# Performance work log

Measured on AMD Instinct MI355X. Metric: run time of the kernel, lower is better.

Reference implementation:

```python
import jax, jax.numpy as jnp
import numpy as np

N, E, G, L = 100000, 1600000, 2000, 2000
IN, H1, H2, H3, OUT = 128, 64, 32, 16, 16
EPS = 1e-5


def _layernorm(x, g, b):
    m = jnp.mean(x, axis=-1, keepdims=True)
    v = jnp.mean(jnp.square(x - m), axis=-1, keepdims=True)
    return (x - m) * jax.lax.rsqrt(v + EPS) * g + b


def _gcn_block(x, W, b, Wr, br, g, beta, src, dst, deg_inv_sqrt):
    # GCNConv with added self-loops and symmetric normalization (PyG default)
    h = x @ W  # [N, F]
    coef = (deg_inv_sqrt[src] * deg_inv_sqrt[dst])[:, None]  # [E, 1]
    msg = h[src] * coef  # [E, F] -- dominant memory traffic
    agg = jax.ops.segment_sum(msg, dst, num_segments=N)
    agg = agg + h * jnp.square(deg_inv_sqrt)[:, None] + b  # self-loop term + bias
    out = agg + (x @ Wr + br)  # residual projection
    return jax.nn.relu(_layernorm(out, g, beta))


def setup_inputs():
    key = jax.random.key(0)
    ks = jax.random.split(key, 40)
    w = lambda k, i, o: jax.random.normal(k, (i, o), jnp.float32) / np.sqrt(i)
    d = {}
    d['x'] = jax.random.normal(ks[0], (N, IN), jnp.float32)
    d['src'] = jax.random.randint(ks[1], (E,), 0, N, jnp.int32)
    d['dst'] = jax.random.randint(ks[2], (E,), 0, N, jnp.int32)
    d['batch'] = jnp.sort(jax.random.randint(ks[3], (N,), 0, G, jnp.int32))
    d['link_idx'] = jax.random.randint(ks[4], (2, L), 0, G, jnp.int32)
    dims = [(IN, H1), (H1, H2), (H2, H3), (H3, OUT)]
    for i, (fi, fo) in enumerate(dims, 1):
        d[f'W{i}'] = w(ks[5 + 4 * i], fi, fo)
        d[f'b{i}'] = jnp.zeros((fo,), jnp.float32)
        d[f'Wr{i}'] = w(ks[6 + 4 * i], fi, fo)
        d[f'br{i}'] = jnp.zeros((fo,), jnp.float32)
        d[f'g{i}'] = jnp.ones((fo,), jnp.float32)
        d[f'bt{i}'] = jnp.zeros((fo,), jnp.float32)
    d['Wm1'] = w(ks[30], 2 * OUT, OUT)
    d['bm1'] = jnp.zeros((OUT,), jnp.float32)
    d['Wm2'] = w(ks[31], OUT, OUT // 2)
    d['bm2'] = jnp.zeros((OUT // 2,), jnp.float32)
    d['Wm3'] = w(ks[32], OUT // 2, 1)
    d['bm3'] = jnp.zeros((1,), jnp.float32)
    return d


def reference(x, src, dst, batch, link_idx,
              W1, b1, Wr1, br1, g1, bt1,
              W2, b2, Wr2, br2, g2, bt2,
              W3, b3, Wr3, br3, g3, bt3,
              W4, b4, Wr4, br4, g4, bt4,
              Wm1, bm1, Wm2, bm2, Wm3, bm3):
    ones_e = jnp.ones((E,), jnp.float32)
    deg = jax.ops.segment_sum(ones_e, dst, num_segments=N) + 1.0  # + self-loop
    dis = jax.lax.rsqrt(deg)
    h = _gcn_block(x, W1, b1, Wr1, br1, g1, bt1, src, dst, dis)
    h = _gcn_block(h, W2, b2, Wr2, br2, g2, bt2, src, dst, dis)
    h = _gcn_block(h, W3, b3, Wr3, br3, g3, bt3, src, dst, dis)
    h = _gcn_block(h, W4, b4, Wr4, br4, g4, bt4, src, dst, dis)
    # global mean pool over subgraphs
    cnt = jax.ops.segment_sum(jnp.ones((N,), jnp.float32), batch, num_segments=G)
    gemb = jax.ops.segment_sum(h, batch, num_segments=G) / jnp.maximum(cnt, 1.0)[:, None]
    feat = jnp.concatenate([gemb[link_idx[0]], gemb[link_idx[1]]], axis=1)  # [L, 2*OUT]
    z = jax.nn.relu(feat @ Wm1 + bm1)
    z = jax.nn.relu(z @ Wm2 + bm2)
    z = z @ Wm3 + bm3
    return jax.nn.sigmoid(z).squeeze(-1)  # [L]
```

## Files before the change

kernel.cpp:

```cpp
#include <hip/hip_runtime.h>
#include <math.h>

namespace {

constexpr int N = 100000;
constexpr int E = 1600000;
constexpr int G = 2000;
constexpr int L = 2000;

constexpr int SCAN_CHUNK = 1024;
constexpr int NB = (N + SCAN_CHUNK - 1) / SCAN_CHUNK;

constexpr int NXCD = 8;
constexpr int NP = N / NXCD;

__device__ __forceinline__ float bf2f(unsigned short u) {
  union { unsigned int i; float f; } v;
  v.i = ((unsigned int)u) << 16;
  return v.f;
}
__device__ __forceinline__ unsigned short f2bf(float f) {
  union { float f; unsigned int i; } v;
  v.f = f;
  const unsigned int x = v.i;
  return (unsigned short)((x + 0x7FFFu + ((x >> 16) & 1u)) >> 16);
}


__global__ void hist_part_kernel(const int* __restrict__ dst, int* __restrict__ deg) {
  const int part = blockIdx.x & (NXCD - 1);
  const int lo = part * NP;
  const int hi = lo + NP;
  const int bidp = blockIdx.x >> 3;
  const int stridev = (gridDim.x >> 3) * blockDim.x;
  const int nvec = E >> 2;
  for (int v = bidp * blockDim.x + threadIdx.x; v < nvec; v += stridev) {
    const int4 d4 = *reinterpret_cast<const int4*>(dst + v * 4);
    if (d4.x >= lo && d4.x < hi) atomicAdd(&deg[d4.x], 1);
    if (d4.y >= lo && d4.y < hi) atomicAdd(&deg[d4.y], 1);
    if (d4.z >= lo && d4.z < hi) atomicAdd(&deg[d4.z], 1);
    if (d4.w >= lo && d4.w < hi) atomicAdd(&deg[d4.w], 1);
  }
}

__global__ void fill_part_kernel(const int* __restrict__ src, const int* __restrict__ dst,
                                 int* __restrict__ cursor, int* __restrict__ col) {
  const int part = blockIdx.x & (NXCD - 1);
  const int lo = part * NP;
  const int hi = lo + NP;
  const int bidp = blockIdx.x >> 3;
  const int stridev = (gridDim.x >> 3) * blockDim.x;
  const int nvec = E >> 2;
  for (int v = bidp * blockDim.x + threadIdx.x; v < nvec; v += stridev) {
    const int e = v * 4;
    const int4 d4 = *reinterpret_cast<const int4*>(dst + e);
    if (d4.x >= lo && d4.x < hi) col[atomicAdd(&cursor[d4.x], 1)] = src[e];
    if (d4.y >= lo && d4.y < hi) col[atomicAdd(&cursor[d4.y], 1)] = src[e + 1];
    if (d4.z >= lo && d4.z < hi) col[atomicAdd(&cursor[d4.z], 1)] = src[e + 2];
    if (d4.w >= lo && d4.w < hi) col[atomicAdd(&cursor[d4.w], 1)] = src[e + 3];
  }
}

__global__ void scan1_kernel(const int* __restrict__ deg, int* __restrict__ bsum) {
  const int t = threadIdx.x;
  const int base = blockIdx.x * SCAN_CHUNK + t * 4;
  int s = 0;
  if (base < N) {
    const int4 v = *reinterpret_cast<const int4*>(deg + base);
    s = v.x + v.y + v.z + v.w;
  }
  __shared__ int ss[256];
  ss[t] = s;
  __syncthreads();
#pragma unroll
  for (int off = 128; off >= 1; off >>= 1) {
    if (t < off) ss[t] += ss[t + off];
    __syncthreads();
  }
  if (t == 0) bsum[blockIdx.x] = ss[0];
}

__global__ void scan2_kernel(const int* __restrict__ bsum, int* __restrict__ boff) {
  __shared__ int ss[128];
  const int t = threadIdx.x;
  ss[t] = (t < NB) ? bsum[t] : 0;
  __syncthreads();
#pragma unroll
  for (int off = 1; off < 128; off <<= 1) {
    int v = (t >= off) ? ss[t - off] : 0;
    __syncthreads();
    ss[t] += v;
    __syncthreads();
  }
  if (t < NB) boff[t] = (t == 0) ? 0 : ss[t - 1];
}

__global__ void scan3_kernel(const int* __restrict__ deg, const int* __restrict__ boff,
                             int* __restrict__ row_ptr, int* __restrict__ cursor,
                             float* __restrict__ dis) {
  const int t = threadIdx.x;
  const int base = blockIdx.x * SCAN_CHUNK + t * 4;
  int d0 = 0, d1 = 0, d2 = 0, d3 = 0;
  if (base < N) {
    const int4 v = *reinterpret_cast<const int4*>(deg + base);
    d0 = v.x; d1 = v.y; d2 = v.z; d3 = v.w;
  }
  const int tsum = d0 + d1 + d2 + d3;
  __shared__ int ss[256];
  ss[t] = tsum;
  __syncthreads();
#pragma unroll
  for (int off = 1; off < 256; off <<= 1) {
    int v = (t >= off) ? ss[t - off] : 0;
    __syncthreads();
    ss[t] += v;
    __syncthreads();
  }
  if (base < N) {
    const int p0 = ((t == 0) ? 0 : ss[t - 1]) + boff[blockIdx.x];
    const int p1 = p0 + d0;
    const int p2 = p1 + d1;
    const int p3 = p2 + d2;
    *reinterpret_cast<int4*>(row_ptr + base) = make_int4(p0, p1, p2, p3);
    *reinterpret_cast<int4*>(cursor + base) = make_int4(p0, p1, p2, p3);
    const float4 dv = make_float4(rsqrtf((float)d0 + 1.0f), rsqrtf((float)d1 + 1.0f),
                                  rsqrtf((float)d2 + 1.0f), rsqrtf((float)d3 + 1.0f));
    *reinterpret_cast<float4*>(dis + base) = dv;
  }
  if (blockIdx.x == 0 && t == 0) row_ptr[N] = E;
}


__device__ __forceinline__ void f4fma(float4& a, float s, const float4 w) {
  a.x = fmaf(s, w.x, a.x);
  a.y = fmaf(s, w.y, a.y);
  a.z = fmaf(s, w.z, a.z);
  a.w = fmaf(s, w.w, a.w);
}

template <int FI, int FO>
__global__ __launch_bounds__(1024) void gemm2_kernel(const float* __restrict__ x,
                                                     const float* __restrict__ W,
                                                     const float* __restrict__ Wr,
                                                     const float* __restrict__ dis,
                                                     unsigned short* __restrict__ hdb,
                                                     float* __restrict__ r) {
  __shared__ float sW[FI * FO];
  __shared__ float sWr[FI * FO];
  for (int i = threadIdx.x; i < FI * FO; i += blockDim.x) {
    sW[i] = W[i];
    sWr[i] = Wr[i];
  }
  __syncthreads();
  constexpr int CG = FO / 4;
  const int total = (N / 4) * CG;
  const int stride = gridDim.x * blockDim.x;
  for (int idx = blockIdx.x * blockDim.x + threadIdx.x; idx < total; idx += stride) {
    const int rb = idx / CG;
    const int col = (idx - rb * CG) * 4;
    const int row0 = rb * 4;
    float4 aH[4], aR[4];
#pragma unroll
    for (int i = 0; i < 4; ++i) {
      aH[i] = make_float4(0.f, 0.f, 0.f, 0.f);
      aR[i] = make_float4(0.f, 0.f, 0.f, 0.f);
    }
    const float* xr = x + (size_t)row0 * FI;
#pragma unroll
    for (int k = 0; k < FI; k += 4) {
      float xs[4][4];
#pragma unroll
      for (int i = 0; i < 4; ++i) {
        const float4 xv = *reinterpret_cast<const float4*>(xr + i * FI + k);
        xs[i][0] = xv.x; xs[i][1] = xv.y; xs[i][2] = xv.z; xs[i][3] = xv.w;
      }
#pragma unroll
      for (int kk = 0; kk < 4; ++kk) {
        const float4 w4 = *reinterpret_cast<const float4*>(&sW[(k + kk) * FO + col]);
        const float4 w4r = *reinterpret_cast<const float4*>(&sWr[(k + kk) * FO + col]);
#pragma unroll
        for (int i = 0; i < 4; ++i) {
          f4fma(aH[i], xs[i][kk], w4);
          f4fma(aR[i], xs[i][kk], w4r);
        }
      }
    }
    const float4 dv = *reinterpret_cast<const float4*>(dis + row0);
    const float dl[4] = {dv.x, dv.y, dv.z, dv.w};
#pragma unroll
    for (int i = 0; i < 4; ++i) {
      ushort4 ob;
      ob.x = f2bf(aH[i].x * dl[i]);
      ob.y = f2bf(aH[i].y * dl[i]);
      ob.z = f2bf(aH[i].z * dl[i]);
      ob.w = f2bf(aH[i].w * dl[i]);
      *reinterpret_cast<ushort4*>(&hdb[(size_t)(row0 + i) * FO + col]) = ob;
      *reinterpret_cast<float4*>(&r[(size_t)(row0 + i) * FO + col]) = aR[i];
    }
  }
}


template <int FO, bool POOL>
__global__ void gcn_agg_kernel(const int* __restrict__ row_ptr, const int* __restrict__ col,
                               const unsigned short* __restrict__ hdb, const float* __restrict__ r,
                               const float* __restrict__ dis,
                               const float* __restrict__ b, const float* __restrict__ br,
                               const float* __restrict__ g, const float* __restrict__ bt,
                               float* __restrict__ out, const int* __restrict__ batch,
                               float* __restrict__ gemb, float* __restrict__ cnt) {
  constexpr int NPW = 64 / FO;
  const int lane = threadIdx.x & 63;
  const int f = lane & (FO - 1);
  const int sub = lane / FO;
  const int waveId = (blockIdx.x * blockDim.x + threadIdx.x) >> 6;
  const int nWaves = (gridDim.x * blockDim.x) >> 6;
  const int nGroups = N / NPW;
  const float bf = b[f], brf = br[f], gf = g[f], btf = bt[f];
  for (int w = waveId; w < nGroups; w += nWaves) {
    const int node = w * NPW + sub;
    const int beg = row_ptr[node];
    const int end = row_ptr[node + 1];
    float a0 = 0.f, a1 = 0.f, a2 = 0.f, a3 = 0.f;
    int k = beg;
    const int end4 = beg + ((end - beg) & ~3);
    for (; k < end4; k += 4) {
      const int s0 = col[k];
      const int s1 = col[k + 1];
      const int s2 = col[k + 2];
      const int s3 = col[k + 3];
      a0 += bf2f(hdb[(size_t)s0 * FO + f]);
      a1 += bf2f(hdb[(size_t)s1 * FO + f]);
      a2 += bf2f(hdb[(size_t)s2 * FO + f]);
      a3 += bf2f(hdb[(size_t)s3 * FO + f]);
    }
    for (; k < end; ++k) a0 += bf2f(hdb[(size_t)col[k] * FO + f]);
    const float acc = (a0 + a1) + (a2 + a3);
    const float dv = dis[node];
    const size_t base = (size_t)node * FO + f;
    const float v = fmaf(dv, acc + bf2f(hdb[base]), bf + r[base] + brf);
    float s = v;
#pragma unroll
    for (int m = FO / 2; m >= 1; m >>= 1) s += __shfl_xor(s, m, 64);
    const float mean = s * (1.0f / FO);
    const float d0 = v - mean;
    float vs = d0 * d0;
#pragma unroll
    for (int m = FO / 2; m >= 1; m >>= 1) vs += __shfl_xor(vs, m, 64);
    const float var = vs * (1.0f / FO);
    float o = d0 * rsqrtf(var + 1e-5f) * gf + btf;
    o = fmaxf(o, 0.f);
    if (POOL) {
      const int bb = batch[node];
      atomicAdd(&gemb[bb * FO + f], o);
      if (f == 0) atomicAdd(&cnt[bb], 1.0f);
    } else {
      out[base] = o;
    }
  }
}


__global__ void gdiv_kernel(float* __restrict__ gemb, const float* __restrict__ cnt) {
  const int idx = blockIdx.x * blockDim.x + threadIdx.x;
  if (idx < G * 16) gemb[idx] /= fmaxf(cnt[idx >> 4], 1.0f);
}

__global__ void mlp_kernel(const float* __restrict__ gemb, const int* __restrict__ link,
                           const float* __restrict__ Wm1, const float* __restrict__ bm1,
                           const float* __restrict__ Wm2, const float* __restrict__ bm2,
                           const float* __restrict__ Wm3, const float* __restrict__ bm3,
                           float* __restrict__ out) {
  __shared__ float sW1[32 * 16], sW2[16 * 8], sW3[8], sb1[16], sb2[8], sb3;
  for (int i = threadIdx.x; i < 32 * 16; i += blockDim.x) sW1[i] = Wm1[i];
  for (int i = threadIdx.x; i < 16 * 8; i += blockDim.x) sW2[i] = Wm2[i];
  if (threadIdx.x < 8) {
    sW3[threadIdx.x] = Wm3[threadIdx.x];
    sb2[threadIdx.x] = bm2[threadIdx.x];
  }
  if (threadIdx.x < 16) sb1[threadIdx.x] = bm1[threadIdx.x];
  if (threadIdx.x == 0) sb3 = bm3[0];
  __syncthreads();
  const int l = blockIdx.x * blockDim.x + threadIdx.x;
  if (l >= L) return;
  const int a = link[l];
  const int c = link[L + l];
  float feat[32];
#pragma unroll
  for (int k = 0; k < 16; ++k) feat[k] = gemb[a * 16 + k];
#pragma unroll
  for (int k = 0; k < 16; ++k) feat[16 + k] = gemb[c * 16 + k];
  float z1[16];
#pragma unroll
  for (int j = 0; j < 16; ++j) {
    float s = sb1[j];
#pragma unroll
    for (int k = 0; k < 32; ++k) s = fmaf(feat[k], sW1[k * 16 + j], s);
    z1[j] = fmaxf(s, 0.f);
  }
  float z2[8];
#pragma unroll
  for (int j = 0; j < 8; ++j) {
    float s = sb2[j];
#pragma unroll
    for (int k = 0; k < 16; ++k) s = fmaf(z1[k], sW2[k * 8 + j], s);
    z2[j] = fmaxf(s, 0.f);
  }
  float z3 = sb3;
#pragma unroll
  for (int k = 0; k < 8; ++k) z3 = fmaf(z2[k], sW3[k], z3);
  out[l] = 1.f / (1.f + expf(-z3));
}

}

extern "C" void kernel_launch(void* const* d_in, const int* in_sizes, int n_in,
                              void* d_out, int out_size, void* d_ws, size_t ws_size,
                              hipStream_t stream) {
  (void)in_sizes; (void)n_in; (void)out_size; (void)ws_size;
  const float* x = (const float*)d_in[0];
  const int* src = (const int*)d_in[1];
  const int* dst = (const int*)d_in[2];
  const int* batch = (const int*)d_in[3];
  const int* link = (const int*)d_in[4];
  const float *Wl[4], *bl[4], *Wrl[4], *brl[4], *gl[4], *btl[4];
  for (int i = 0; i < 4; ++i) {
    Wl[i] = (const float*)d_in[5 + 6 * i + 0];
    bl[i] = (const float*)d_in[5 + 6 * i + 1];
    Wrl[i] = (const float*)d_in[5 + 6 * i + 2];
    brl[i] = (const float*)d_in[5 + 6 * i + 3];
    gl[i] = (const float*)d_in[5 + 6 * i + 4];
    btl[i] = (const float*)d_in[5 + 6 * i + 5];
  }
  const float* Wm1 = (const float*)d_in[29];
  const float* bm1 = (const float*)d_in[30];
  const float* Wm2 = (const float*)d_in[31];
  const float* bm2 = (const float*)d_in[32];
  const float* Wm3 = (const float*)d_in[33];
  const float* bm3 = (const float*)d_in[34];
  float* out = (float*)d_out;

  char* wsb = (char*)d_ws;
  int* deg_i = (int*)wsb;
  int* row_ptr = deg_i + N;
  int* cursor = row_ptr + (N + 1);
  float* dis = (float*)(cursor + N);
  int* bsum = (int*)(dis + N);
  int* boff = bsum + NB;
  int* col = boff + NB;
  unsigned short* hdb = (unsigned short*)(col + E);
  float* bufB = (float*)(hdb + (size_t)N * 64);
  float* bufC = bufB + (size_t)N * 64;
  float* gemb = bufC + (size_t)N * 64;
  float* cnt = gemb + (size_t)G * 16;

  hipMemsetAsync(deg_i, 0, N * sizeof(int), stream);
  hist_part_kernel<<<2048, 256, 0, stream>>>(dst, deg_i);
  scan1_kernel<<<NB, 256, 0, stream>>>(deg_i, bsum);
  scan2_kernel<<<1, 128, 0, stream>>>(bsum, boff);
  scan3_kernel<<<NB, 256, 0, stream>>>(deg_i, boff, row_ptr, cursor, dis);
  fill_part_kernel<<<2048, 256, 0, stream>>>(src, dst, cursor, col);

  const int AGG_BLOCKS = 2048;

  gemm2_kernel<128, 64><<<((N / 4) * 16 + 1023) / 1024, 1024, 0, stream>>>(x, Wl[0], Wrl[0], dis, hdb, bufB);
  gcn_agg_kernel<64, false><<<AGG_BLOCKS, 256, 0, stream>>>(row_ptr, col, hdb, bufB, dis,
                                                            bl[0], brl[0], gl[0], btl[0], bufC,
                                                            batch, gemb, cnt);
  gemm2_kernel<64, 32><<<((N / 4) * 8 + 1023) / 1024, 1024, 0, stream>>>(bufC, Wl[1], Wrl[1], dis, hdb, bufB);
  gcn_agg_kernel<32, false><<<AGG_BLOCKS, 256, 0, stream>>>(row_ptr, col, hdb, bufB, dis,
                                                            bl[1], brl[1], gl[1], btl[1], bufC,
                                                            batch, gemb, cnt);
  gemm2_kernel<32, 16><<<((N / 4) * 4 + 1023) / 1024, 1024, 0, stream>>>(bufC, Wl[2], Wrl[2], dis, hdb, bufB);
  gcn_agg_kernel<16, false><<<AGG_BLOCKS, 256, 0, stream>>>(row_ptr, col, hdb, bufB, dis,
                                                            bl[2], brl[2], gl[2], btl[2], bufC,
                                                            batch, gemb, cnt);
  hipMemsetAsync(gemb, 0, (size_t)(G * 16 + G) * sizeof(float), stream);
  gemm2_kernel<16, 16><<<((N / 4) * 4 + 1023) / 1024, 1024, 0, stream>>>(bufC, Wl[3], Wrl[3], dis, hdb, bufB);
  gcn_agg_kernel<16, true><<<AGG_BLOCKS, 256, 0, stream>>>(row_ptr, col, hdb, bufB, dis,
                                                           bl[3], brl[3], gl[3], btl[3], nullptr,
                                                           batch, gemb, cnt);
  gdiv_kernel<<<(G * 16 + 255) / 256, 256, 0, stream>>>(gemb, cnt);
  mlp_kernel<<<(L + 255) / 256, 256, 0, stream>>>(gemb, link, Wm1, bm1, Wm2, bm2, Wm3, bm3, out);
}
```

Measured before the change: 628.3 us.

## Fuse scan kernels cooperatively, fold pool zeroing and divide, unroll gather by 8

Merges the three-stage degree scan into one cooperative kernel that uses grid syncs, and moves the pool-buffer memset into the last GEMM kernel. It also folds the mean-pool division into the MLP kernel, removing several launches. Separately, the aggregation gather loop is unrolled to 8 with clamped indices and predicated adds, putting more loads in flight. The cooperative launch and grid syncs add their own overhead, and the clamped loads issue redundant memory reads for the tail of each neighbour list.

```diff
diff --git a/kernel.cpp b/kernel.cpp
--- a/kernel.cpp
+++ b/kernel.cpp
@@ -1,5 +1,8 @@
 #include <hip/hip_runtime.h>
+#include <hip/hip_cooperative_groups.h>
 #include <math.h>
+
+namespace cg = cooperative_groups;
 
 namespace {
 
@@ -61,63 +64,60 @@
   }
 }
 
-__global__ void scan1_kernel(const int* __restrict__ deg, int* __restrict__ bsum) {
-  const int t = threadIdx.x;
-  const int base = blockIdx.x * SCAN_CHUNK + t * 4;
-  int s = 0;
-  if (base < N) {
-    const int4 v = *reinterpret_cast<const int4*>(deg + base);
-    s = v.x + v.y + v.z + v.w;
-  }
+__global__ __launch_bounds__(256) void scan_fused_kernel(const int* __restrict__ deg,
+                                                         int* __restrict__ bsum,
+                                                         int* __restrict__ boff,
+                                                         int* __restrict__ row_ptr,
+                                                         int* __restrict__ cursor,
+                                                         float* __restrict__ dis) {
+  cg::grid_group grid = cg::this_grid();
+  const int tid = threadIdx.x;
+  const int bid = blockIdx.x;
+  const int base = bid * SCAN_CHUNK + tid * 4;
   __shared__ int ss[256];
-  ss[t] = s;
-  __syncthreads();
-#pragma unroll
-  for (int off = 128; off >= 1; off >>= 1) {
-    if (t < off) ss[t] += ss[t + off];
-    __syncthreads();
-  }
-  if (t == 0) bsum[blockIdx.x] = ss[0];
-}
-
-__global__ void scan2_kernel(const int* __restrict__ bsum, int* __restrict__ boff) {
-  __shared__ int ss[128];
-  const int t = threadIdx.x;
-  ss[t] = (t < NB) ? bsum[t] : 0;
-  __syncthreads();
-#pragma unroll
-  for (int off = 1; off < 128; off <<= 1) {
-    int v = (t >= off) ? ss[t - off] : 0;
-    __syncthreads();
-    ss[t] += v;
-    __syncthreads();
-  }
-  if (t < NB) boff[t] = (t == 0) ? 0 : ss[t - 1];
-}
-
-__global__ void scan3_kernel(const int* __restrict__ deg, const int* __restrict__ boff,
-                             int* __restrict__ row_ptr, int* __restrict__ cursor,
-                             float* __restrict__ dis) {
-  const int t = threadIdx.x;
-  const int base = blockIdx.x * SCAN_CHUNK + t * 4;
+
   int d0 = 0, d1 = 0, d2 = 0, d3 = 0;
   if (base < N) {
     const int4 v = *reinterpret_cast<const int4*>(deg + base);
     d0 = v.x; d1 = v.y; d2 = v.z; d3 = v.w;
   }
-  const int tsum = d0 + d1 + d2 + d3;
-  __shared__ int ss[256];
-  ss[t] = tsum;
+  ss[tid] = d0 + d1 + d2 + d3;
   __syncthreads();
 #pragma unroll
+  for (int off = 128; off >= 1; off >>= 1) {
+    if (tid < off) ss[tid] += ss[tid + off];
+    __syncthreads();
+  }
+  if (tid == 0) bsum[bid] = ss[0];
+  grid.sync();
+
+  if (bid == 0) {
+    __shared__ int s2[256];
+    s2[tid] = (tid < NB) ? bsum[tid] : 0;
+    __syncthreads();
+#pragma unroll
+    for (int off = 1; off < 256; off <<= 1) {
+      const int v = (tid >= off) ? s2[tid - off] : 0;
+      __syncthreads();
+      s2[tid] += v;
+      __syncthreads();
+    }
+    if (tid < NB) boff[tid] = (tid == 0) ? 0 : s2[tid - 1];
+  }
+  grid.sync();
+
+  __syncthreads();
+  ss[tid] = d0 + d1 + d2 + d3;
+  __syncthreads();
+#pragma unroll
   for (int off = 1; off < 256; off <<= 1) {
-    int v = (t >= off) ? ss[t - off] : 0;
+    const int v = (tid >= off) ? ss[tid - off] : 0;
     __syncthreads();
-    ss[t] += v;
+    ss[tid] += v;
     __syncthreads();
   }
   if (base < N) {
-    const int p0 = ((t == 0) ? 0 : ss[t - 1]) + boff[blockIdx.x];
+    const int p0 = ((tid == 0) ? 0 : ss[tid - 1]) + boff[bid];
     const int p1 = p0 + d0;
     const int p2 = p1 + d1;
     const int p3 = p2 + d2;
@@ -127,7 +127,7 @@
                                   rsqrtf((float)d2 + 1.0f), rsqrtf((float)d3 + 1.0f));
     *reinterpret_cast<float4*>(dis + base) = dv;
   }
-  if (blockIdx.x == 0 && t == 0) row_ptr[N] = E;
+  if (bid == 0 && tid == 0) row_ptr[N] = E;
 }
 
 
@@ -138,18 +138,24 @@
   a.w = fmaf(s, w.w, a.w);
 }
 
-template <int FI, int FO>
+template <int FI, int FO, bool ZERO_POOL>
 __global__ __launch_bounds__(1024) void gemm2_kernel(const float* __restrict__ x,
                                                      const float* __restrict__ W,
                                                      const float* __restrict__ Wr,
                                                      const float* __restrict__ dis,
                                                      unsigned short* __restrict__ hdb,
-                                                     float* __restrict__ r) {
+                                                     float* __restrict__ r,
+                                                     float* __restrict__ gemb_cnt) {
   __shared__ float sW[FI * FO];
   __shared__ float sWr[FI * FO];
   for (int i = threadIdx.x; i < FI * FO; i += blockDim.x) {
     sW[i] = W[i];
     sWr[i] = Wr[i];
+  }
+  if (ZERO_POOL) {
+    const int gstride = gridDim.x * blockDim.x;
+    for (int i = blockIdx.x * blockDim.x + threadIdx.x; i < G * 16 + G; i += gstride)
+      gemb_cnt[i] = 0.f;
   }
   __syncthreads();
   constexpr int CG = FO / 4;
@@ -221,21 +227,31 @@
     const int node = w * NPW + sub;
     const int beg = row_ptr[node];
     const int end = row_ptr[node + 1];
-    float a0 = 0.f, a1 = 0.f, a2 = 0.f, a3 = 0.f;
-    int k = beg;
-    const int end4 = beg + ((end - beg) & ~3);
-    for (; k < end4; k += 4) {
-      const int s0 = col[k];
-      const int s1 = col[k + 1];
-      const int s2 = col[k + 2];
-      const int s3 = col[k + 3];
-      a0 += bf2f(hdb[(size_t)s0 * FO + f]);
-      a1 += bf2f(hdb[(size_t)s1 * FO + f]);
-      a2 += bf2f(hdb[(size_t)s2 * FO + f]);
-      a3 += bf2f(hdb[(size_t)s3 * FO + f]);
-    }
-    for (; k < end; ++k) a0 += bf2f(hdb[(size_t)col[k] * FO + f]);
-    const float acc = (a0 + a1) + (a2 + a3);
+    float a0 = 0.f, a1 = 0.f, a2 = 0.f, a3 = 0.f, a4 = 0.f, a5 = 0.f, a6 = 0.f, a7 = 0.f;
+    for (int k = beg; k < end; k += 8) {
+      const int e1 = end - 1;
+      const int k0 = k, k1 = min(k + 1, e1), k2 = min(k + 2, e1), k3 = min(k + 3, e1);
+      const int k4 = min(k + 4, e1), k5 = min(k + 5, e1), k6 = min(k + 6, e1), k7 = min(k + 7, e1);
+      const int s0 = col[k0], s1 = col[k1], s2 = col[k2], s3 = col[k3];
+      const int s4 = col[k4], s5 = col[k5], s6 = col[k6], s7 = col[k7];
+      const float v0 = bf2f(hdb[(size_t)s0 * FO + f]);
+      const float v1 = bf2f(hdb[(size_t)s1 * FO + f]);
+      const float v2 = bf2f(hdb[(size_t)s2 * FO + f]);
+      const float v3 = bf2f(hdb[(size_t)s3 * FO + f]);
+      const float v4 = bf2f(hdb[(size_t)s4 * FO + f]);
+      const float v5 = bf2f(hdb[(size_t)s5 * FO + f]);
+      const float v6 = bf2f(hdb[(size_t)s6 * FO + f]);
+      const float v7 = bf2f(hdb[(size_t)s7 * FO + f]);
+      a0 += v0;
+      a1 += (k + 1 < end) ? v1 : 0.f;
+      a2 += (k + 2 < end) ? v2 : 0.f;
+      a3 += (k + 3 < end) ? v3 : 0.f;
+      a4 += (k + 4 < end) ? v4 : 0.f;
+      a5 += (k + 5 < end) ? v5 : 0.f;
+      a6 += (k + 6 < end) ? v6 : 0.f;
+      a7 += (k + 7 < end) ? v7 : 0.f;
+    }
+    const float acc = ((a0 + a1) + (a2 + a3)) + ((a4 + a5) + (a6 + a7));
     const float dv = dis[node];
     const size_t base = (size_t)node * FO + f;
     const float v = fmaf(dv, acc + bf2f(hdb[base]), bf + r[base] + brf);
@@ -261,12 +277,8 @@
 }
 
 
-__global__ void gdiv_kernel(float* __restrict__ gemb, const float* __restrict__ cnt) {
-  const int idx = blockIdx.x * blockDim.x + threadIdx.x;
-  if (idx < G * 16) gemb[idx] /= fmaxf(cnt[idx >> 4], 1.0f);
-}
-
-__global__ void mlp_kernel(const float* __restrict__ gemb, const int* __restrict__ link,
+__global__ void mlp_kernel(const float* __restrict__ gemb, const float* __restrict__ cnt,
+                           const int* __restrict__ link,
                            const float* __restrict__ Wm1, const float* __restrict__ bm1,
                            const float* __restrict__ Wm2, const float* __restrict__ bm2,
                            const float* __restrict__ Wm3, const float* __restrict__ bm3,
@@ -285,11 +297,13 @@
   if (l >= L) return;
   const int a = link[l];
   const int c = link[L + l];
+  const float ia = 1.0f / fmaxf(cnt[a], 1.0f);
+  const float ic = 1.0f / fmaxf(cnt[c], 1.0f);
   float feat[32];
 #pragma unroll
-  for (int k = 0; k < 16; ++k) feat[k] = gemb[a * 16 + k];
-#pragma unroll
-  for (int k = 0; k < 16; ++k) feat[16 + k] = gemb[c * 16 + k];
+  for (int k = 0; k < 16; ++k) feat[k] = gemb[a * 16 + k] * ia;
+#pragma unroll
+  for (int k = 0; k < 16; ++k) feat[16 + k] = gemb[c * 16 + k] * ic;
   float z1[16];
 #pragma unroll
   for (int j = 0; j < 16; ++j) {
@@ -356,30 +370,34 @@
 
   hipMemsetAsync(deg_i, 0, N * sizeof(int), stream);
   hist_part_kernel<<<2048, 256, 0, stream>>>(dst, deg_i);
-  scan1_kernel<<<NB, 256, 0, stream>>>(deg_i, bsum);
-  scan2_kernel<<<1, 128, 0, stream>>>(bsum, boff);
-  scan3_kernel<<<NB, 256, 0, stream>>>(deg_i, boff, row_ptr, cursor, dis);
+  {
+    void* args[] = {&deg_i, &bsum, &boff, &row_ptr, &cursor, &dis};
+    hipLaunchCooperativeKernel((void*)scan_fused_kernel, dim3(NB), dim3(256), args, 0, stream);
+  }
   fill_part_kernel<<<2048, 256, 0, stream>>>(src, dst, cursor, col);
 
   const int AGG_BLOCKS = 2048;
 
-  gemm2_kernel<128, 64><<<((N / 4) * 16 + 1023) / 1024, 1024, 0, stream>>>(x, Wl[0], Wrl[0], dis, hdb, bufB);
+  gemm2_kernel<128, 64, false><<<((N / 4) * 16 + 1023) / 1024, 1024, 0, stream>>>(
+      x, Wl[0], Wrl[0], dis, hdb, bufB, nullptr);
   gcn_agg_kernel<64, false><<<AGG_BLOCKS, 256, 0, stream>>>(row_ptr, col, hdb, bufB, dis,
                                                             bl[0], brl[0], gl[0], btl[0], bufC,
                                                             batch, gemb, cnt);
-  gemm2_kernel<64, 32><<<((N / 4) * 8 + 1023) / 1024, 1024, 0, stream>>>(bufC, Wl[1], Wrl[1], dis, hdb, bufB);
+  gemm2_kernel<64, 32, false><<<((N / 4) * 8 + 1023) / 1024, 1024, 0, stream>>>(
+      bufC, Wl[1], Wrl[1], dis, hdb, bufB, nullptr);
   gcn_agg_kernel<32, false><<<AGG_BLOCKS, 256, 0, stream>>>(row_ptr, col, hdb, bufB, dis,
                                                             bl[1], brl[1], gl[1], btl[1], bufC,
                                                             batch, gemb, cnt);
-  gemm2_kernel<32, 16><<<((N / 4) * 4 + 1023) / 1024, 1024, 0, stream>>>(bufC, Wl[2], Wrl[2], dis, hdb, bufB);
+  gemm2_kernel<32, 16, false><<<((N / 4) * 4 + 1023) / 1024, 1024, 0, stream>>>(
+      bufC, Wl[2], Wrl[2], dis, hdb, bufB, nullptr);
   gcn_agg_kernel<16, false><<<AGG_BLOCKS, 256, 0, stream>>>(row_ptr, col, hdb, bufB, dis,
                                                             bl[2], brl[2], gl[2], btl[2], bufC,
                                                             batch, gemb, cnt);
-  hipMemsetAsync(gemb, 0, (size_t)(G * 16 + G) * sizeof(float), stream);
-  gemm2_kernel<16, 16><<<((N / 4) * 4 + 1023) / 1024, 1024, 0, stream>>>(bufC, Wl[3], Wrl[3], dis, hdb, bufB);
+  gemm2_kernel<16, 16, true><<<((N / 4) * 4 + 1023) / 1024, 1024, 0, stream>>>(
+      bufC, Wl[3], Wrl[3], dis, hdb, bufB, gemb);
   gcn_agg_kernel<16, true><<<AGG_BLOCKS, 256, 0, stream>>>(row_ptr, col, hdb, bufB, dis,
                                                            bl[3], brl[3], gl[3], btl[3], nullptr,
                                                            batch, gemb, cnt);
-  gdiv_kernel<<<(G * 16 + 255) / 256, 256, 0, stream>>>(gemb, cnt);
-  mlp_kernel<<<(L + 255) / 256, 256, 0, stream>>>(gemb, link, Wm1, bm1, Wm2, bm2, Wm3, bm3, out);
-}
+  mlp_kernel<<<(L + 255) / 256, 256, 0, stream>>>(gemb, cnt, link, Wm1, bm1, Wm2, bm2, Wm3, bm3,
+                                                  out);
+}
```

Result: slower. 732.2 us (+16.5%).
